# Kernel optimization log

Measured on AMD Instinct MI355X. Metric: run time of the kernel, lower is better.

Reference implementation:

```python
import jax, jax.numpy as jnp
import numpy as np

N_NODES = 50000
N_EDGES = 800000
NF = 64       # input_nf = output_nf = hidden_nf
RADIAL = 1

def tanhshrink(x):
    return x - jnp.tanh(x)

def _linear_params(key, fan_in, fan_out):
    k1, k2 = jax.random.split(key)
    s = 1.0 / np.sqrt(fan_in)
    W = jax.random.uniform(k1, (fan_in, fan_out), jnp.float32, -s, s)
    b = jax.random.uniform(k2, (fan_out,), jnp.float32, -s, s)
    return W, b

def setup_inputs() -> dict:
    key = jax.random.key(0)
    ks = jax.random.split(key, 11)
    nodes = jax.random.normal(ks[0], (N_NODES, NF), jnp.float32)
    coord = jax.random.normal(ks[1], (N_NODES, 3), jnp.float32)
    edges = jax.random.randint(ks[2], (2, N_EDGES), 0, N_NODES, jnp.int64)
    # Edge MLP: Linear(2*NF + RADIAL -> NF), Linear(NF -> NF)
    eW1, eb1 = _linear_params(ks[3], 2 * NF + RADIAL, NF)
    eW2, eb2 = _linear_params(ks[4], NF, NF)
    # Edge attention: Linear(2*NF -> NF), Linear(NF -> 1)
    aW1, ab1 = _linear_params(ks[5], 2 * NF, NF)
    aW2, ab2 = _linear_params(ks[6], NF, 1)
    # Node MLP: Linear(NF + NF -> NF), Linear(NF -> NF)
    nW1, nb1 = _linear_params(ks[7], 2 * NF, NF)
    nW2, nb2 = _linear_params(ks[8], NF, NF)
    # Coord MLP: Linear(NF -> NF), Linear(NF -> 1)
    cW1, cb1 = _linear_params(ks[9], NF, NF)
    cW2, cb2 = _linear_params(ks[10], NF, 1)
    return dict(nodes=nodes, coord=coord, edges=edges,
                eW1=eW1, eb1=eb1, eW2=eW2, eb2=eb2,
                aW1=aW1, ab1=ab1, aW2=aW2, ab2=ab2,
                nW1=nW1, nb1=nb1, nW2=nW2, nb2=nb2,
                cW1=cW1, cb1=cb1, cW2=cW2, cb2=cb2)

def reference(nodes, coord, edges,
              eW1, eb1, eW2, eb2,
              aW1, ab1, aW2, ab2,
              nW1, nb1, nW2, nb2,
              cW1, cb1, cW2, cb2):
    row, col = edges[0], edges[1]
    n = nodes.shape[0]
    # Radial: squared distance along each edge
    rij = coord[row] - coord[col]                       # [E, 3]
    radial = jnp.sum(rij * rij, axis=1, keepdims=True)  # [E, 1]
    src, tgt = nodes[row], nodes[col]                   # [E, NF]
    # Edge MLP with attention gate
    agg_in = jnp.concatenate([src, tgt, radial], axis=1)
    h = tanhshrink(agg_in @ eW1 + eb1)
    h = tanhshrink(h @ eW2 + eb2)                       # [E, NF]
    att_in = jnp.concatenate([src, tgt], axis=1)
    a = tanhshrink(att_in @ aW1 + ab1)
    a = jax.nn.sigmoid(a @ aW2 + ab2)                   # [E, 1]
    edge_feat = h * a                                   # [E, NF]
    # Coordinate update: rij scaled by scalar per edge, scatter-add to row
    c = tanhshrink(edge_feat @ cW1 + cb1)
    trans = rij * (c @ cW2 + cb2)                       # [E, 3]
    coord_out = coord + jax.ops.segment_sum(trans, row, num_segments=n)
    # Node update: scatter-add edge features to row, residual MLP
    agg = jax.ops.segment_sum(edge_feat, row, num_segments=n)  # [N, NF]
    m = jnp.concatenate([nodes, agg], axis=1)
    m = tanhshrink(m @ nW1 + nb1)
    nodes_out = nodes + (m @ nW2 + nb2)
    return nodes_out, coord_out
```

## Files before the change

### kernel.cpp

```cpp
#include <hip/hip_runtime.h>
#include <hip/hip_fp16.h>

#define NF 64

typedef _Float16 half8 __attribute__((ext_vector_type(8)));
typedef float f32x4 __attribute__((ext_vector_type(4)));

__device__ __forceinline__ float ts_f(float x){
  float t = __expf(2.0f*x);
  float th = 1.0f - 2.0f*__builtin_amdgcn_rcpf(t + 1.0f);
  return x - th;
}
__device__ __forceinline__ float sigmoid_f(float x){
  return __builtin_amdgcn_rcpf(1.0f + __expf(-x));
}

__global__ __launch_bounds__(256) void k_prepw_hist(
    const float* __restrict__ eW1, const float* __restrict__ aW1,
    const float* __restrict__ eW2, const float* __restrict__ cW1,
    const float* __restrict__ nW1, const float* __restrict__ nW2,
    _Float16* __restrict__ W256t, _Float16* __restrict__ N1t,
    _Float16* __restrict__ W2t, _Float16* __restrict__ C1t,
    _Float16* __restrict__ N2t,
    const int* __restrict__ edges, int* __restrict__ counts,
    int* __restrict__ rank, int E)
{
  const int bi = blockIdx.x;
  if (bi < 64){
    const int t = bi*256 + threadIdx.x;
    {
      const int n = t >> 6, k = t & 63;
      float v;
      if      (n < 64)  v = eW1[k*NF + n];
      else if (n < 128) v = aW1[k*NF + (n-64)];
      else if (n < 192) v = eW1[(64+k)*NF + (n-128)];
      else              v = aW1[(64+k)*NF + (n-192)];
      W256t[t] = (_Float16)v;
    }
    if (t < 64*128){
      const int n = t >> 7, k = t & 127;
      N1t[t] = (_Float16)nW1[k*NF + n];
    }
    if (t < 64*64){
      const int n = t >> 6, k = t & 63;
      W2t[t] = (_Float16)eW2[k*NF + n];
      C1t[t] = (_Float16)cW1[k*NF + n];
      N2t[t] = (_Float16)nW2[k*NF + n];
    }
  } else {
    const int e = (bi - 64)*256 + threadIdx.x;
    if (e < E) rank[e] = atomicAdd(&counts[edges[e]], 1);
  }
}

__global__ __launch_bounds__(256) void k_scan_zero(
    const int* __restrict__ counts, int* __restrict__ offs,
    int* __restrict__ btot, int* __restrict__ btop, int* __restrict__ done,
    const int* __restrict__ sentinel,
    float4* __restrict__ zagg, int naggf4,
    float4* __restrict__ zcoord, int ncoordf4,
    int SCAN_B)
{
  const int t = threadIdx.x;
  const int b = blockIdx.x;
  if (b >= SCAN_B){
    const float4 z = make_float4(0.f,0.f,0.f,0.f);
    const int nthr = (gridDim.x - SCAN_B) * 256;
    const int tid = (b - SCAN_B)*256 + t;
    for (int i = tid; i < naggf4; i += nthr)   zagg[i] = z;
    for (int i = tid; i < ncoordf4; i += nthr) zcoord[i] = z;
    return;
  }

  __shared__ int s[256];
  __shared__ int isLast;
  const int BASE = *sentinel;
  const int4 c = *(const int4*)(counts + b*1024 + 4*t);
  const int c0 = c.x - BASE, c1 = c.y - BASE, c2 = c.z - BASE, c3 = c.w - BASE;
  const int mysum = c0 + c1 + c2 + c3;
  s[t] = mysum; __syncthreads();
  #pragma unroll
  for (int d=1; d<256; d<<=1){
    const int v = (t>=d) ? s[t-d] : 0; __syncthreads();
    s[t] += v; __syncthreads();
  }
  const int base = (t==0) ? 0 : s[t-1];
  int4 o;
  o.x = base; o.y = base + c0; o.z = o.y + c1; o.w = o.z + c2;
  *(int4*)(offs + b*1024 + 4*t) = o;
  if (t == 255) btot[b] = s[255];

  __threadfence();
  if (t == 0) isLast = (atomicAdd(done, 1) == BASE + SCAN_B - 1);
  __syncthreads();
  if (isLast){
    __threadfence();
    const int v = (t < SCAN_B) ? btot[t] : 0;
    s[t] = v; __syncthreads();
    #pragma unroll
    for (int d=1; d<256; d<<=1){
      const int u = (t>=d) ? s[t-d] : 0; __syncthreads();
      s[t] += u; __syncthreads();
    }
    if (t < SCAN_B) btop[t] = (t==0) ? 0 : s[t-1];
  }
}

__global__ __launch_bounds__(64, 8) void k_pre_scatter(
    const float* __restrict__ nodes,
    const float* __restrict__ eb1, const float* __restrict__ ab1,
    const _Float16* __restrict__ W256t,
    _Float16* __restrict__ P, _Float16* __restrict__ Q, int N,
    const int* __restrict__ edges, const int* __restrict__ offs,
    const int* __restrict__ btop, const int* __restrict__ rank,
    const int* __restrict__ sentinel,
    int* __restrict__ rs, int* __restrict__ cs, int E,
    int preBlocks)
{
  const int bi = blockIdx.x;
  const int lane = threadIdx.x;
  if (bi >= preBlocks){
    const int BASE = *sentinel;
    const int e = (bi - preBlocks)*64 + lane;
    if (e < E){
      const int r = edges[e], c = edges[E + e];
      const int pos = btop[r >> 10] + offs[r] + (rank[e] - BASE);
      rs[pos] = r; cs[pos] = c;
    }
    return;
  }

  const int p = lane & 15, q = lane >> 4;
  const int m0 = bi * 16;
  const int row = m0 + p;

  const float* __restrict__ xr = nodes + (size_t)row * NF;
  half8 A[2];
  #pragma unroll
  for (int kt=0; kt<2; kt++){
    const float4 xa = *(const float4*)(xr + kt*32 + q*8);
    const float4 xb = *(const float4*)(xr + kt*32 + q*8 + 4);
    A[kt][0]=(_Float16)xa.x; A[kt][1]=(_Float16)xa.y; A[kt][2]=(_Float16)xa.z; A[kt][3]=(_Float16)xa.w;
    A[kt][4]=(_Float16)xb.x; A[kt][5]=(_Float16)xb.y; A[kt][6]=(_Float16)xb.z; A[kt][7]=(_Float16)xb.w;
  }

  #pragma unroll
  for (int ni=0; ni<16; ni++){
    float b = 0.f;
    if (ni < 4)       b = eb1[16*ni + p];
    else if (ni < 8)  b = ab1[16*(ni-4) + p];
    f32x4 acc = (f32x4){b,b,b,b};
    #pragma unroll
    for (int kt=0; kt<2; kt++){
      const half8 Bf = *(const half8*)(W256t + (size_t)(16*ni + p)*NF + kt*32 + q*8);
      acc = __builtin_amdgcn_mfma_f32_16x16x32_f16(A[kt], Bf, acc, 0,0,0);
    }
    _Float16* __restrict__ dst = (ni < 8 ? P : Q);
    const int colbase = (ni & 7) * 16 + p;
    #pragma unroll
    for (int rr=0; rr<4; rr++)
      dst[(size_t)(m0 + 4*q + rr)*128 + colbase] = (_Float16)acc[rr];
  }
}

__global__ __launch_bounds__(64, 4) void egcl_edge(
    const float* __restrict__ coord,
    const int*   __restrict__ rs, const int* __restrict__ cs,
    const _Float16* __restrict__ P, const _Float16* __restrict__ Q,
    const float* __restrict__ eW1,
    const _Float16* __restrict__ W2t, const float* __restrict__ eb2,
    const float* __restrict__ aW2, const float* __restrict__ ab2,
    const _Float16* __restrict__ C1t, const float* __restrict__ cb1,
    const float* __restrict__ cW2, const float* __restrict__ cb2,
    _Float16* __restrict__ aggh, float* __restrict__ coord_out,
    int E)
{
  __shared__ _Float16 tile[64][72];
  __shared__ float gcbuf[64];

  const int lane = threadIdx.x;
  const int p = lane & 15, q = lane >> 4;
  const int e = blockIdx.x * 64 + lane;
  const bool valid = (e < E);
  const int el = valid ? e : (E - 1);

  const int r = rs[el];
  const int c = cs[el];
  *(int*)&tile[lane][70] = valid ? r : -1;

  const float rx = coord[3*r+0] - coord[3*c+0];
  const float ry = coord[3*r+1] - coord[3*c+1];
  const float rz = coord[3*r+2] - coord[3*c+2];
  const float radial = rx*rx + ry*ry + rz*rz;

  const _Float16* __restrict__ Pr = P + (size_t)r * 128;
  const _Float16* __restrict__ Qc = Q + (size_t)c * 128;
  const float* __restrict__ wrad = eW1 + 128*NF;

  half8 Bf[4][2];
  #pragma unroll
  for (int ni=0;ni<4;ni++)
    #pragma unroll
    for (int kt=0;kt<2;kt++)
      Bf[ni][kt] = *(const half8*)(W2t + (size_t)(16*ni + p)*NF + kt*32 + q*8);

  float sp0=0.f, sp1=0.f;
  #pragma unroll
  for (int g=0;g<8;g++){
    const half8 pa = *(const half8*)(Pr + 64 + 8*g);
    const half8 qa = *(const half8*)(Qc + 64 + 8*g);
    #pragma unroll
    for (int j=0;j<8;j++){
      const float v = ts_f((float)pa[j] + (float)qa[j]);
      if (j & 1) sp1 = fmaf(v, aW2[8*g+j], sp1); else sp0 = fmaf(v, aW2[8*g+j], sp0);
    }
  }
  const float gate = sigmoid_f(sp0 + sp1 + ab2[0]);
  gcbuf[lane] = gate;

  #pragma unroll
  for (int g=0;g<8;g++){
    const half8 ph = *(const half8*)(Pr + 8*g);
    const half8 qh = *(const half8*)(Qc + 8*g);
    half8 hv;
    #pragma unroll
    for (int j=0;j<8;j++)
      hv[j] = (_Float16)ts_f(fmaf(radial, wrad[8*g+j], (float)ph[j] + (float)qh[j]));
    *(half8*)&tile[lane][8*g] = hv;
  }
  __syncthreads();

  f32x4 acc[4][4];
  #pragma unroll
  for (int ni=0;ni<4;ni++){
    const float b = eb2[16*ni + p];
    #pragma unroll
    for (int mi=0;mi<4;mi++) acc[mi][ni] = (f32x4){b,b,b,b};
  }
  #pragma unroll
  for (int mi=0;mi<4;mi++){
    #pragma unroll
    for (int kt=0;kt<2;kt++){
      const half8 Af = *(const half8*)&tile[16*mi + p][kt*32 + q*8];
      #pragma unroll
      for (int ni=0;ni<4;ni++)
        acc[mi][ni] = __builtin_amdgcn_mfma_f32_16x16x32_f16(Af, Bf[ni][kt], acc[mi][ni], 0,0,0);
    }
  }
  __syncthreads();

  #pragma unroll
  for (int mi=0;mi<4;mi++){
    #pragma unroll
    for (int rr=0;rr<4;rr++){
      const int row = 16*mi + 4*q + rr;
      const float gv = gcbuf[row];
      #pragma unroll
      for (int ni=0;ni<4;ni++)
        tile[row][16*ni + p] = (_Float16)(ts_f(acc[mi][ni][rr]) * gv);
    }
  }

  #pragma unroll
  for (int ni=0;ni<4;ni++)
    #pragma unroll
    for (int kt=0;kt<2;kt++)
      Bf[ni][kt] = *(const half8*)(C1t + (size_t)(16*ni + p)*NF + kt*32 + q*8);
  #pragma unroll
  for (int ni=0;ni<4;ni++){
    const float b = cb1[16*ni + p];
    #pragma unroll
    for (int mi=0;mi<4;mi++) acc[mi][ni] = (f32x4){b,b,b,b};
  }
  __syncthreads();
  #pragma unroll
  for (int mi=0;mi<4;mi++){
    #pragma unroll
    for (int kt=0;kt<2;kt++){
      const half8 Af = *(const half8*)&tile[16*mi + p][kt*32 + q*8];
      #pragma unroll
      for (int ni=0;ni<4;ni++)
        acc[mi][ni] = __builtin_amdgcn_mfma_f32_16x16x32_f16(Af, Bf[ni][kt], acc[mi][ni], 0,0,0);
    }
  }

  float part[4][4];
  {
    float w2c[4];
    #pragma unroll
    for (int ni=0;ni<4;ni++) w2c[ni] = cW2[16*ni + p];
    #pragma unroll
    for (int mi=0;mi<4;mi++)
      #pragma unroll
      for (int rr=0;rr<4;rr++){
        float s = 0.f;
        #pragma unroll
        for (int ni=0;ni<4;ni++) s = fmaf(ts_f(acc[mi][ni][rr]), w2c[ni], s);
        part[mi][rr] = s;
      }
  }
  #pragma unroll
  for (int mask=1; mask<16; mask<<=1)
    #pragma unroll
    for (int mi=0;mi<4;mi++)
      #pragma unroll
      for (int rr=0;rr<4;rr++)
        part[mi][rr] += __shfl_xor(part[mi][rr], mask);
  {
    float v = 0.f;
    #pragma unroll
    for (int mi=0;mi<4;mi++)
      #pragma unroll
      for (int rr=0;rr<4;rr++)
        if (((p>>2)==mi) & ((p&3)==rr)) v = part[mi][rr];
    gcbuf[16*(p>>2) + 4*q + (p&3)] = v + cb2[0];
  }
  __syncthreads();

  {
    const float cse = gcbuf[lane];
    float* tb = (float*)&tile[lane][64];
    tb[0] = rx * cse;
    tb[1] = ry * cse;
    tb[2] = rz * cse;
  }
  __syncthreads();

  {
    int cur = __builtin_amdgcn_readfirstlane(*(const int*)&tile[0][70]);
    float runsum = 0.f, rc = 0.f;
    #pragma unroll 1
    for (int eo=0; eo<64; eo++){
      const int rr2 = __builtin_amdgcn_readfirstlane(*(const int*)&tile[eo][70]);
      if (rr2 != cur){
        const float v0 = __shfl(runsum, 2*lane);
        const float v1 = __shfl(runsum, 2*lane+1);
        if (cur >= 0){
          if (lane < 32){
            __half2 hv; hv.x = __float2half(v0); hv.y = __float2half(v1);
            unsafeAtomicAdd((__half2*)aggh + (size_t)cur*32 + lane, hv);
          }
          if (lane < 3) atomicAdd(coord_out + 3*cur + lane, rc);
        }
        runsum = 0.f; rc = 0.f; cur = rr2;
      }
      runsum += (float)tile[eo][lane];
      if (lane < 3) rc += ((const float*)&tile[eo][64])[lane];
    }
    const float v0 = __shfl(runsum, 2*lane);
    const float v1 = __shfl(runsum, 2*lane+1);
    if (cur >= 0){
      if (lane < 32){
        __half2 hv; hv.x = __float2half(v0); hv.y = __float2half(v1);
        unsafeAtomicAdd((__half2*)aggh + (size_t)cur*32 + lane, hv);
      }
      if (lane < 3) atomicAdd(coord_out + 3*cur + lane, rc);
    }
  }
}

__global__ __launch_bounds__(64, 8) void egcl_node(
    const float* __restrict__ nodes, const float* __restrict__ coord,
    const _Float16* __restrict__ aggh,
    const _Float16* __restrict__ N1t, const float* __restrict__ nb1,
    const _Float16* __restrict__ N2t, const float* __restrict__ nb2,
    float* __restrict__ out_nodes, float* __restrict__ out_coord, int N)
{
  __shared__ _Float16 t2[16][72];
  const int lane = threadIdx.x;
  const int p = lane & 15, q = lane >> 4;
  const int m0 = blockIdx.x * 16;
  const int row = m0 + p;

  half8 A[4];
  const float* __restrict__ xr = nodes + (size_t)row * NF;
  #pragma unroll
  for (int kt=0; kt<2; kt++){
    const float4 xa = *(const float4*)(xr + kt*32 + q*8);
    const float4 xb = *(const float4*)(xr + kt*32 + q*8 + 4);
    A[kt][0]=(_Float16)xa.x; A[kt][1]=(_Float16)xa.y; A[kt][2]=(_Float16)xa.z; A[kt][3]=(_Float16)xa.w;
    A[kt][4]=(_Float16)xb.x; A[kt][5]=(_Float16)xb.y; A[kt][6]=(_Float16)xb.z; A[kt][7]=(_Float16)xb.w;
  }
  const _Float16* __restrict__ ar = aggh + (size_t)row * NF;
  #pragma unroll
  for (int kt=2; kt<4; kt++)
    A[kt] = *(const half8*)(ar + (kt-2)*32 + q*8);

  f32x4 acc[4];
  #pragma unroll
  for (int ni=0;ni<4;ni++){
    const float b = nb1[16*ni + p];
    acc[ni] = (f32x4){b,b,b,b};
  }
  #pragma unroll
  for (int kt=0; kt<4; kt++){
    #pragma unroll
    for (int ni=0;ni<4;ni++){
      const half8 Bf = *(const half8*)(N1t + (size_t)(16*ni + p)*128 + kt*32 + q*8);
      acc[ni] = __builtin_amdgcn_mfma_f32_16x16x32_f16(A[kt], Bf, acc[ni], 0,0,0);
    }
  }

  #pragma unroll
  for (int ni=0;ni<4;ni++)
    #pragma unroll
    for (int rr=0;rr<4;rr++)
      t2[4*q + rr][16*ni + p] = (_Float16)ts_f(acc[ni][rr]);
  __syncthreads();

  half8 A2[2];
  #pragma unroll
  for (int kt=0; kt<2; kt++)
    A2[kt] = *(const half8*)&t2[p][kt*32 + q*8];

  f32x4 acc2[4];
  #pragma unroll
  for (int ni=0;ni<4;ni++){
    const float b = nb2[16*ni + p];
    acc2[ni] = (f32x4){b,b,b,b};
  }
  #pragma unroll
  for (int kt=0; kt<2; kt++){
    #pragma unroll
    for (int ni=0;ni<4;ni++){
      const half8 Bf = *(const half8*)(N2t + (size_t)(16*ni + p)*NF + kt*32 + q*8);
      acc2[ni] = __builtin_amdgcn_mfma_f32_16x16x32_f16(A2[kt], Bf, acc2[ni], 0,0,0);
    }
  }

  #pragma unroll
  for (int ni=0;ni<4;ni++){
    #pragma unroll
    for (int rr=0;rr<4;rr++){
      const size_t idx = (size_t)(m0 + 4*q + rr)*NF + 16*ni + p;
      out_nodes[idx] = nodes[idx] + acc2[ni][rr];
    }
  }

  if (lane < 48)
    out_coord[(size_t)m0*3 + lane] += coord[(size_t)m0*3 + lane];
}

extern "C" void kernel_launch(void* const* d_in, const int* in_sizes, int n_in,
                              void* d_out, int out_size, void* d_ws, size_t ws_size,
                              hipStream_t stream)
{
  const float* nodes = (const float*)d_in[0];
  const float* coord = (const float*)d_in[1];
  const int*   edges = (const int*)  d_in[2];
  const float* eW1 = (const float*)d_in[3];
  const float* eb1 = (const float*)d_in[4];
  const float* eW2 = (const float*)d_in[5];
  const float* eb2 = (const float*)d_in[6];
  const float* aW1 = (const float*)d_in[7];
  const float* ab1 = (const float*)d_in[8];
  const float* aW2 = (const float*)d_in[9];
  const float* ab2 = (const float*)d_in[10];
  const float* nW1 = (const float*)d_in[11];
  const float* nb1 = (const float*)d_in[12];
  const float* nW2 = (const float*)d_in[13];
  const float* nb2 = (const float*)d_in[14];
  const float* cW1 = (const float*)d_in[15];
  const float* cb1 = (const float*)d_in[16];
  const float* cW2 = (const float*)d_in[17];
  const float* cb2 = (const float*)d_in[18];

  const int E = in_sizes[2] / 2;
  const int N = in_sizes[0] / NF;
  const int SCAN_B = (N + 1023) >> 10;
  const int NBINS  = SCAN_B << 10;
  float* out_nodes = (float*)d_out;
  float* out_coord = out_nodes + (size_t)N * NF;

  char* w = (char*)d_ws;
  _Float16* P     = (_Float16*)w;  w += (size_t)N * 128 * 2;
  _Float16* Qh    = (_Float16*)w;  w += (size_t)N * 128 * 2;
  _Float16* aggh  = (_Float16*)w;  w += (size_t)N * 64 * 2;
  int* counts     = (int*)w;       w += (size_t)NBINS * 4;
  int* done       = (int*)w;       w += 64;
  int* sentinel   = (int*)w;       w += 64;
  int* offs       = (int*)w;       w += (size_t)NBINS * 4;
  int* btot       = (int*)w;       w += 256*4;
  int* btop       = (int*)w;       w += 256*4;
  int* rank       = (int*)w;       w += (size_t)E * 4;
  int* rs         = (int*)w;       w += (size_t)E * 4;
  int* cs_        = (int*)w;       w += (size_t)E * 4;
  _Float16* W256t = (_Float16*)w;  w += 256*64*2;
  _Float16* N1t   = (_Float16*)w;  w += 64*128*2;
  _Float16* W2t   = (_Float16*)w;  w += 64*64*2;
  _Float16* C1t   = (_Float16*)w;  w += 64*64*2;
  _Float16* N2t   = (_Float16*)w;  w += 64*64*2;

  const int histB = (E + 255)/256;
  k_prepw_hist<<<64 + histB, 256, 0, stream>>>(eW1, aW1, eW2, cW1, nW1, nW2,
      W256t, N1t, W2t, C1t, N2t, edges, counts, rank, E);

  const int naggf4   = (int)((size_t)N * 64 * 2 / 16);
  const int ncoordf4 = (N * 3) / 4;
  k_scan_zero<<<SCAN_B + 256, 256, 0, stream>>>(counts, offs, btot, btop, done,
      sentinel, (float4*)aggh, naggf4, (float4*)out_coord, ncoordf4, SCAN_B);

  const int preBlocks = (N + 15)/16;
  const int scatBlocks = (E + 63)/64;
  k_pre_scatter<<<preBlocks + scatBlocks, 64, 0, stream>>>(nodes, eb1, ab1, W256t,
      P, Qh, N, edges, offs, btop, rank, sentinel, rs, cs_, E, preBlocks);

  egcl_edge<<<(E + 63)/64, 64, 0, stream>>>(coord, rs, cs_, P, Qh,
      eW1, W2t, eb2, aW2, ab2, C1t, cb1, cW2, cb2,
      aggh, out_coord, E);

  egcl_node<<<(N + 15)/16, 64, 0, stream>>>(nodes, coord, aggh,
      N1t, nb1, N2t, nb2, out_nodes, out_coord, N);
}
```

Baseline: 303.5 us.

## Use wavefront ballot and segmented scan for edge scatter reduction

Replaces the LDS round-trip for row ids and coordinate translations with a ballot of segment boundaries plus a shuffle-based segmented prefix scan over the 64 edges in the wave. This removes one __syncthreads and the serial per-edge coord accumulation. The feature-sum loop is fully unrolled with batched LDS reads, and it branches on the precomputed boundary mask instead of re-reading row ids each step. The cost is more shuffle instructions per block and a larger unrolled loop body.

```diff
diff --git a/kernel.cpp b/kernel.cpp
--- a/kernel.cpp
+++ b/kernel.cpp
@@ -186,7 +186,7 @@
 
   const int r = rs[el];
   const int c = cs[el];
-  *(int*)&tile[lane][70] = valid ? r : -1;
+  const int rv = valid ? r : -1;
 
   const float rx = coord[3*r+0] - coord[3*c+0];
   const float ry = coord[3*r+1] - coord[3*c+1];
@@ -317,44 +317,64 @@
   }
   __syncthreads();
 
+  const float cse = gcbuf[lane];
+
+  unsigned long long bmask;
   {
-    const float cse = gcbuf[lane];
-    float* tb = (float*)&tile[lane][64];
-    tb[0] = rx * cse;
-    tb[1] = ry * cse;
-    tb[2] = rz * cse;
-  }
-  __syncthreads();
+    const int rvp = __shfl_up(rv, 1);
+    const int fl = (lane == 0) || (rv != rvp);
+    bmask = __ballot(fl);
+  }
 
   {
-    int cur = __builtin_amdgcn_readfirstlane(*(const int*)&tile[0][70]);
-    float runsum = 0.f, rc = 0.f;
-    #pragma unroll 1
-    for (int eo=0; eo<64; eo++){
-      const int rr2 = __builtin_amdgcn_readfirstlane(*(const int*)&tile[eo][70]);
-      if (rr2 != cur){
-        const float v0 = __shfl(runsum, 2*lane);
-        const float v1 = __shfl(runsum, 2*lane+1);
-        if (cur >= 0){
-          if (lane < 32){
+    float tx = rx * cse, ty = ry * cse, tz = rz * cse;
+    int f = (int)((bmask >> lane) & 1ull);
+    #pragma unroll
+    for (int d=1; d<64; d<<=1){
+      const float ux = __shfl_up(tx, d);
+      const float uy = __shfl_up(ty, d);
+      const float uz = __shfl_up(tz, d);
+      const int   g  = __shfl_up(f, d);
+      if (lane >= d && !f){ tx += ux; ty += uy; tz += uz; }
+      if (lane >= d) f |= g;
+    }
+    const int tail = (lane == 63) || (((bmask >> ((lane + 1) & 63)) & 1ull) && lane < 63);
+    if (tail && rv >= 0){
+      atomicAdd(coord_out + 3*rv + 0, tx);
+      atomicAdd(coord_out + 3*rv + 1, ty);
+      atomicAdd(coord_out + 3*rv + 2, tz);
+    }
+  }
+
+  {
+    int cur_r = __shfl(rv, 0);
+    float runsum = 0.f;
+    #pragma unroll
+    for (int g8=0; g8<8; ++g8){
+      _Float16 v[8];
+      #pragma unroll
+      for (int i=0;i<8;i++) v[i] = tile[g8*8 + i][lane];
+      #pragma unroll
+      for (int i=0;i<8;i++){
+        const int eo = g8*8 + i;
+        if (eo > 0 && ((bmask >> eo) & 1ull)){
+          const float v0 = __shfl(runsum, 2*lane);
+          const float v1 = __shfl(runsum, 2*lane+1);
+          if (cur_r >= 0 && lane < 32){
             __half2 hv; hv.x = __float2half(v0); hv.y = __float2half(v1);
-            unsafeAtomicAdd((__half2*)aggh + (size_t)cur*32 + lane, hv);
+            unsafeAtomicAdd((__half2*)aggh + (size_t)cur_r*32 + lane, hv);
           }
-          if (lane < 3) atomicAdd(coord_out + 3*cur + lane, rc);
+          runsum = 0.f;
+          cur_r = __shfl(rv, eo);
         }
-        runsum = 0.f; rc = 0.f; cur = rr2;
+        runsum += (float)v[i];
       }
-      runsum += (float)tile[eo][lane];
-      if (lane < 3) rc += ((const float*)&tile[eo][64])[lane];
     }
     const float v0 = __shfl(runsum, 2*lane);
     const float v1 = __shfl(runsum, 2*lane+1);
-    if (cur >= 0){
-      if (lane < 32){
-        __half2 hv; hv.x = __float2half(v0); hv.y = __float2half(v1);
-        unsafeAtomicAdd((__half2*)aggh + (size_t)cur*32 + lane, hv);
-      }
-      if (lane < 3) atomicAdd(coord_out + 3*cur + lane, rc);
+    if (cur_r >= 0 && lane < 32){
+      __half2 hv; hv.x = __float2half(v0); hv.y = __float2half(v1);
+      unsafeAtomicAdd((__half2*)aggh + (size_t)cur_r*32 + lane, hv);
     }
   }
 }
```

Measured after the change: 295.6 us. 2.6% less time.
